# Kernel tuning notes

Hardware: AMD Instinct MI355X
Metric: run time of the kernel (lower is better)

The kernel has to match this reference:

```python
import jax, jax.numpy as jnp
import numpy as np

B, N, D, H = 64, 257, 1024, 16
HD = D // H  # 64


def setup_inputs() -> dict:
    key = jax.random.key(0)
    k1, k2, k3, k4, k5, k6 = jax.random.split(key, 6)
    x = jax.random.normal(k1, (B, N, D), dtype=jnp.float32)
    # boolean key mask per batch; never mask CLS token (col 0) so no fully-masked rows
    mask = jax.random.randint(k2, (B, N), 0, 2) > 0
    mask = mask.at[:, 0].set(False)
    s = 1.0 / np.sqrt(D)
    in_proj_w = jax.random.normal(k3, (3 * D, D), dtype=jnp.float32) * s
    in_proj_b = jax.random.normal(k4, (3 * D,), dtype=jnp.float32) * 0.02
    out_proj_w = jax.random.normal(k5, (D, D), dtype=jnp.float32) * s
    out_proj_b = jax.random.normal(k6, (D,), dtype=jnp.float32) * 0.02
    return {"x": x, "mask": mask, "in_proj_w": in_proj_w, "in_proj_b": in_proj_b,
            "out_proj_w": out_proj_w, "out_proj_b": out_proj_b}


def reference(x, mask, in_proj_w, in_proj_b, out_proj_w, out_proj_b):
    b, n, d = x.shape
    h, hd = H, d // H
    # fused QKV projection: [b, n, 3*d]
    qkv = jnp.einsum('bnd,ed->bne', x, in_proj_w) + in_proj_b
    # einops 'b n (qkv h d) -> qkv b h n d'
    qkv = qkv.reshape(b, n, 3, h, hd).transpose(2, 0, 3, 1, 4)
    q, k, v = qkv[0], qkv[1], qkv[2]  # each [b, h, n, hd]
    attn_weights = jnp.einsum('bhqe,bhke->bhqk', q, k) / jnp.sqrt(jnp.asarray(hd, x.dtype))
    # mode == 'mask': -inf on masked keys (broadcast over heads and queries)
    attn_weights = jnp.where(mask[:, None, None, :], -jnp.inf, attn_weights)
    attn_matrix = jax.nn.softmax(attn_weights, axis=-1)
    out = jnp.einsum('bhqk,bhke->bhqe', attn_matrix, v)  # [b, h, n, hd]
    out = out.transpose(0, 2, 1, 3).reshape(b, n, d)      # 'b h n d -> b n (h d)'
    return jnp.einsum('bnd,ed->bne', out, out_proj_w) + out_proj_b
```

## Files before the change

kernel.cpp:

```cpp
#include <hip/hip_runtime.h>

#define B_   64
#define N_   257
#define D_   1024
#define H_   16
#define HD_  64
#define M_   (B_*N_)
#define CK_  96
#define VTS_ 128
#define PLS_ 104

typedef __bf16 bf16x8 __attribute__((ext_vector_type(8)));
typedef __bf16 bf16x4 __attribute__((ext_vector_type(4)));
typedef float  f32x4  __attribute__((ext_vector_type(4)));

__device__ __forceinline__ void gload_lds16(const void* g, void* l) {
    __builtin_amdgcn_global_load_lds(
        (const __attribute__((address_space(1))) void*)g,
        (__attribute__((address_space(3))) void*)l, 16, 0, 0);
}

#define XQ_  4210688
#define W1Q_ 786432
#define W2Q_ 262144
__global__ __launch_bounds__(256) void cvt_all(const float* __restrict__ x,
                                               const float* __restrict__ w1,
                                               const float* __restrict__ w2,
                                               __bf16* __restrict__ xb,
                                               __bf16* __restrict__ w1b,
                                               __bf16* __restrict__ w2b) {
    int i = blockIdx.x * 256 + threadIdx.x;
    const float* src; __bf16* dst; int j;
    if (i < XQ_) { src = x; dst = xb; j = i; }
    else if (i < XQ_ + W1Q_) { src = w1; dst = w1b; j = i - XQ_; }
    else if (i < XQ_ + W1Q_ + W2Q_) { src = w2; dst = w2b; j = i - XQ_ - W1Q_; }
    else return;
    float4 v = reinterpret_cast<const float4*>(src)[j];
    bf16x4 o;
    o[0] = (__bf16)v.x; o[1] = (__bf16)v.y; o[2] = (__bf16)v.z; o[3] = (__bf16)v.w;
    *reinterpret_cast<bf16x4*>(dst + (size_t)j * 4) = o;
}

__global__ __launch_bounds__(256) void qkv_gemm(const __bf16* __restrict__ A,
                                                const __bf16* __restrict__ W,
                                                const float* __restrict__ bias,
                                                __bf16* __restrict__ qw,
                                                __bf16* __restrict__ kw,
                                                __bf16* __restrict__ vw) {
    __shared__ __align__(16) char smem[32768];
    __bf16* As = (__bf16*)smem;
    __bf16* Ws = (__bf16*)(smem + 16384);
    __bf16* Ct = (__bf16*)smem;
    const int bid = blockIdx.x;
    int rowt, colt;
    if (bid < 3072) {
        const int xcd = bid & 7, idx = bid >> 3;
        colt = idx >> 4;
        rowt = xcd * 16 + (idx & 15);
    } else {
        rowt = 128; colt = bid - 3072;
    }
    const int row0 = rowt * 128, col0 = colt * 128;
    const int tid  = threadIdx.x;
    const int lane = tid & 63, wv = tid >> 6;
    const int wm = (wv >> 1) * 64, wn = (wv & 1) * 64;
    const int fr = lane & 15, fq = lane >> 4;
    size_t sA[4], sW[4];
#pragma unroll
    for (int i = 0; i < 4; ++i) {
        const int c = tid + i * 256;
        const int r = c >> 3, g = (c & 7) ^ (r & 7);
        sA[i] = (size_t)(row0 + r) * 1024 + g * 8;
        sW[i] = (size_t)(col0 + r) * 1024 + g * 8;
    }
    f32x4 acc[4][4] = {};
    for (int k0 = 0; k0 < 1024; k0 += 64) {
#pragma unroll
        for (int i = 0; i < 4; ++i) {
            gload_lds16(A + sA[i] + k0, (char*)As + i * 4096 + wv * 1024);
            gload_lds16(W + sW[i] + k0, (char*)Ws + i * 4096 + wv * 1024);
        }
        __syncthreads();
#pragma unroll
        for (int ks = 0; ks < 2; ++ks) {
            const int goff = (((ks * 4 + fq) ^ (fr & 7)) * 8);
            bf16x8 af[4], bw[4];
#pragma unroll
            for (int i = 0; i < 4; ++i)
                af[i] = *reinterpret_cast<const bf16x8*>(&As[(wm + i * 16 + fr) * 64 + goff]);
#pragma unroll
            for (int j = 0; j < 4; ++j)
                bw[j] = *reinterpret_cast<const bf16x8*>(&Ws[(wn + j * 16 + fr) * 64 + goff]);
#pragma unroll
            for (int i = 0; i < 4; ++i)
#pragma unroll
                for (int j = 0; j < 4; ++j)
                    acc[i][j] = __builtin_amdgcn_mfma_f32_16x16x32_bf16(af[i], bw[j], acc[i][j], 0, 0, 0);
        }
        __syncthreads();
    }
    const int which = col0 >> 10;
    __bf16* dst = which == 0 ? qw : (which == 1 ? kw : vw);
    const float scale = which == 0 ? 0.125f : 1.0f;
    float bj[4];
#pragma unroll
    for (int j = 0; j < 4; ++j) bj[j] = bias[col0 + wn + j * 16 + fr];
#pragma unroll
    for (int i = 0; i < 4; ++i)
#pragma unroll
        for (int r = 0; r < 4; ++r) {
            const int row = wm + i * 16 + fq * 4 + r;
#pragma unroll
            for (int j = 0; j < 4; ++j)
                Ct[row * 128 + wn + j * 16 + fr] = (__bf16)((acc[i][j][r] + bj[j]) * scale);
        }
    __syncthreads();
    const int h0 = (col0 >> 6) & 15;
    const int col = (tid & 15) * 8;
    const int h = h0 + (col >> 6), hd = col & 63;
#pragma unroll
    for (int p = 0; p < 8; ++p) {
        const int row = p * 16 + (tid >> 4);
        const int m = row0 + row;
        if (m < M_) {
            bf16x8 v = *reinterpret_cast<const bf16x8*>(&Ct[row * 128 + col]);
            const int bb = m / 257, nn = m - bb * 257;
            *reinterpret_cast<bf16x8*>(dst + ((size_t)(bb * 16 + h) * 257 + nn) * 64 + hd) = v;
        }
    }
}

__global__ __launch_bounds__(256) void attn_kernel(const __bf16* __restrict__ qw,
                                                   const __bf16* __restrict__ kw,
                                                   const __bf16* __restrict__ vw,
                                                   const int* __restrict__ mask,
                                                   __bf16* __restrict__ attn) {
    const int bh = blockIdx.x;
    const int bb = bh >> 4, hh = bh & 15;
    const int q0 = blockIdx.y * 64;
    const int tid = threadIdx.x, lane = tid & 63, wv = tid >> 6;
    const int fr = lane & 15, fq = lane >> 4;
    const float NEG_INF = -__builtin_inff();

    __shared__ __align__(16) __bf16 Qs[64 * 64];
    __shared__ __align__(16) __bf16 Ks[CK_ * 64];
    __shared__ __align__(16) __bf16 Vt[64 * VTS_];
    __shared__ __align__(16) __bf16 Pl[4][16 * PLS_];
    __shared__ float maskb[288];

    const __bf16* qg = qw + ((size_t)bh * 257 + q0) * 64;
    const __bf16* kg = kw + (size_t)bh * 257 * 64;
    const __bf16* vg = vw + (size_t)bh * 257 * 64;
    const int* mg = mask + bb * 257;

    for (int idx = tid; idx < 288; idx += 256)
        maskb[idx] = (idx < 257 && mg[idx] == 0) ? 0.0f : NEG_INF;

#pragma unroll
    for (int i = 0; i < 2; ++i) {
        const int c = tid + i * 256;
        const int r = c >> 3, g = (c & 7) ^ (r & 7);
        gload_lds16(qg + (size_t)r * 64 + g * 8, (char*)Qs + i * 4096 + wv * 1024);
    }

    float m_run[4] = {NEG_INF, NEG_INF, NEG_INF, NEG_INF};
    float l_run[4] = {};
    f32x4 Oa[4] = {};

    for (int c3 = 0; c3 < 3; ++c3) {
        const int k0 = c3 * CK_;
        __syncthreads();
#pragma unroll
        for (int i = 0; i < 3; ++i) {
            const int c = tid + i * 256;
            const int r = c >> 3, g = (c & 7) ^ (r & 7);
            if (k0 + r < 257)
                gload_lds16(kg + (size_t)(k0 + r) * 64 + g * 8, (char*)Ks + i * 4096 + wv * 1024);
        }
#pragma unroll
        for (int it = 0; it < 3; ++it) {
            const int t = tid + it * 256;
            const int key = t >> 3, grp = t & 7;
            if (k0 + key < 257) {
                bf16x8 v8 = *reinterpret_cast<const bf16x8*>(vg + (size_t)(k0 + key) * 64 + grp * 8);
#pragma unroll
                for (int u = 0; u < 8; ++u) {
                    const int hd = grp * 8 + u;
                    Vt[hd * VTS_ + (((key >> 3) ^ (hd & 7)) * 8) + (key & 7)] = v8[u];
                }
            }
        }
        __syncthreads();

        f32x4 s[6];
        {
            bf16x8 aq[2];
#pragma unroll
            for (int ks = 0; ks < 2; ++ks)
                aq[ks] = *reinterpret_cast<const bf16x8*>(
                    &Qs[(wv * 16 + fr) * 64 + (((ks * 4 + fq) ^ (fr & 7)) * 8)]);
#pragma unroll
            for (int nt = 0; nt < 6; ++nt) {
                f32x4 sa = {};
#pragma unroll
                for (int ks = 0; ks < 2; ++ks) {
                    bf16x8 bk = *reinterpret_cast<const bf16x8*>(
                        &Ks[(nt * 16 + fr) * 64 + (((ks * 4 + fq) ^ (fr & 7)) * 8)]);
                    sa = __builtin_amdgcn_mfma_f32_16x16x32_bf16(aq[ks], bk, sa, 0, 0, 0);
                }
                const float mb = maskb[k0 + nt * 16 + fr];
#pragma unroll
                for (int r = 0; r < 4; ++r) sa[r] += mb;
                s[nt] = sa;
            }
        }
        float alpha[4];
#pragma unroll
        for (int r = 0; r < 4; ++r) {
            float v = s[0][r];
#pragma unroll
            for (int nt = 1; nt < 6; ++nt) v = fmaxf(v, s[nt][r]);
            v = fmaxf(v, __shfl_xor(v, 1));
            v = fmaxf(v, __shfl_xor(v, 2));
            v = fmaxf(v, __shfl_xor(v, 4));
            v = fmaxf(v, __shfl_xor(v, 8));
            const float mnew = fmaxf(m_run[r], v);
            alpha[r] = __expf(m_run[r] - mnew);
            m_run[r] = mnew;
        }
        float sm[4] = {};
#pragma unroll
        for (int nt = 0; nt < 6; ++nt)
#pragma unroll
            for (int r = 0; r < 4; ++r) {
                const float p = __expf(s[nt][r] - m_run[r]);
                s[nt][r] = p;
                sm[r] += p;
            }
#pragma unroll
        for (int r = 0; r < 4; ++r) {
            float v = sm[r];
            v += __shfl_xor(v, 1);
            v += __shfl_xor(v, 2);
            v += __shfl_xor(v, 4);
            v += __shfl_xor(v, 8);
            l_run[r] = l_run[r] * alpha[r] + v;
        }
#pragma unroll
        for (int ot = 0; ot < 4; ++ot)
#pragma unroll
            for (int r = 0; r < 4; ++r) Oa[ot][r] *= alpha[r];
#pragma unroll
        for (int nt = 0; nt < 6; ++nt)
#pragma unroll
            for (int r = 0; r < 4; ++r)
                Pl[wv][(fq * 4 + r) * PLS_ + nt * 16 + fr] = (__bf16)s[nt][r];
        __syncthreads();
        bf16x8 ap[3];
#pragma unroll
        for (int kk = 0; kk < 3; ++kk)
            ap[kk] = *reinterpret_cast<const bf16x8*>(&Pl[wv][fr * PLS_ + kk * 32 + fq * 8]);
#pragma unroll
        for (int ot = 0; ot < 4; ++ot) {
            const int row = ot * 16 + fr;
#pragma unroll
            for (int kk = 0; kk < 3; ++kk) {
                bf16x8 bv = *reinterpret_cast<const bf16x8*>(
                    &Vt[row * VTS_ + (((kk * 4 + fq) ^ (fr & 7)) * 8)]);
                Oa[ot] = __builtin_amdgcn_mfma_f32_16x16x32_bf16(ap[kk], bv, Oa[ot], 0, 0, 0);
            }
        }
    }
#pragma unroll
    for (int r = 0; r < 4; ++r) {
        const int n = q0 + wv * 16 + fq * 4 + r;
        const float inv = 1.0f / l_run[r];
#pragma unroll
        for (int ot = 0; ot < 4; ++ot)
            attn[((size_t)(bb * 257 + n)) * 1024 + hh * 64 + ot * 16 + fr] =
                (__bf16)(Oa[ot][r] * inv);
    }
}

__global__ __launch_bounds__(320) void attn_tail(const __bf16* __restrict__ qw,
                                                 const __bf16* __restrict__ kw,
                                                 const __bf16* __restrict__ vw,
                                                 const int* __restrict__ mask,
                                                 __bf16* __restrict__ attn) {
    const int bh = blockIdx.x;
    const int bb = bh >> 4, hh = bh & 15;
    const int tid = threadIdx.x, wv = tid >> 6;
    const float NEG_INF = -__builtin_inff();
    __shared__ float pbuf[257];
    __shared__ float red[5];
    __shared__ float gstat[2];

    const __bf16* qg = qw + ((size_t)bh * 257 + 256) * 64;
    const __bf16* kg = kw + (size_t)bh * 257 * 64;
    const __bf16* vg = vw + (size_t)bh * 257 * 64;

    float s = NEG_INF;
    if (tid < 257) {
        const __bf16* kr = kg + (size_t)tid * 64;
        float acc = 0.0f;
#pragma unroll
        for (int g = 0; g < 8; ++g) {
            bf16x8 qv = *reinterpret_cast<const bf16x8*>(qg + g * 8);
            bf16x8 kv = *reinterpret_cast<const bf16x8*>(kr + g * 8);
#pragma unroll
            for (int u = 0; u < 8; ++u) acc += (float)qv[u] * (float)kv[u];
        }
        s = (mask[bb * 257 + tid] == 0) ? acc : NEG_INF;
    }
    float v = s;
#pragma unroll
    for (int d = 1; d < 64; d <<= 1) v = fmaxf(v, __shfl_xor(v, d));
    if ((tid & 63) == 0) red[wv] = v;
    __syncthreads();
    if (tid == 0) {
        float m = red[0];
#pragma unroll
        for (int w = 1; w < 5; ++w) m = fmaxf(m, red[w]);
        gstat[0] = m;
    }
    __syncthreads();
    const float gmax = gstat[0];
    float p = (tid < 257) ? __expf(s - gmax) : 0.0f;
    if (tid < 257) pbuf[tid] = p;
    float sv = p;
#pragma unroll
    for (int d = 1; d < 64; d <<= 1) sv += __shfl_xor(sv, d);
    if ((tid & 63) == 0) red[wv] = sv;
    __syncthreads();
    if (tid == 0) gstat[1] = red[0] + red[1] + red[2] + red[3] + red[4];
    __syncthreads();
    if (tid < 64) {
        const float inv = 1.0f / gstat[1];
        float o = 0.0f;
        for (int j = 0; j < 257; ++j)
            o += pbuf[j] * (float)vg[(size_t)j * 64 + tid];
        attn[((size_t)(bb * 257 + 256)) * 1024 + hh * 64 + tid] = (__bf16)(o * inv);
    }
}

__global__ __launch_bounds__(256) void out_gemm(const __bf16* __restrict__ A,
                                                const __bf16* __restrict__ W,
                                                const float* __restrict__ bias,
                                                float* __restrict__ out) {
    __shared__ __align__(16) char smem[32768];
    __bf16* As = (__bf16*)smem;
    __bf16* Ws = (__bf16*)(smem + 16384);
    const int bid = blockIdx.x;
    int rowt, colt;
    if (bid < 1024) {
        const int xcd = bid & 7, idx = bid >> 3;
        colt = idx >> 4;
        rowt = xcd * 16 + (idx & 15);
    } else {
        rowt = 128; colt = bid - 1024;
    }
    const int row0 = rowt * 128, col0 = colt * 128;
    const int tid  = threadIdx.x;
    const int lane = tid & 63, wv = tid >> 6;
    const int wm = (wv >> 1) * 64, wn = (wv & 1) * 64;
    const int fr = lane & 15, fq = lane >> 4;
    size_t sA[4], sW[4];
#pragma unroll
    for (int i = 0; i < 4; ++i) {
        const int c = tid + i * 256;
        const int r = c >> 3, g = (c & 7) ^ (r & 7);
        sA[i] = (size_t)(row0 + r) * 1024 + g * 8;
        sW[i] = (size_t)(col0 + r) * 1024 + g * 8;
    }
    f32x4 acc[4][4] = {};
    for (int k0 = 0; k0 < 1024; k0 += 64) {
#pragma unroll
        for (int i = 0; i < 4; ++i) {
            gload_lds16(A + sA[i] + k0, (char*)As + i * 4096 + wv * 1024);
            gload_lds16(W + sW[i] + k0, (char*)Ws + i * 4096 + wv * 1024);
        }
        __syncthreads();
#pragma unroll
        for (int ks = 0; ks < 2; ++ks) {
            const int goff = (((ks * 4 + fq) ^ (fr & 7)) * 8);
            bf16x8 af[4], bw[4];
#pragma unroll
            for (int i = 0; i < 4; ++i)
                af[i] = *reinterpret_cast<const bf16x8*>(&As[(wm + i * 16 + fr) * 64 + goff]);
#pragma unroll
            for (int j = 0; j < 4; ++j)
                bw[j] = *reinterpret_cast<const bf16x8*>(&Ws[(wn + j * 16 + fr) * 64 + goff]);
#pragma unroll
            for (int i = 0; i < 4; ++i)
#pragma unroll
                for (int j = 0; j < 4; ++j)
                    acc[i][j] = __builtin_amdgcn_mfma_f32_16x16x32_bf16(af[i], bw[j], acc[i][j], 0, 0, 0);
        }
        __syncthreads();
    }
    float bj[4];
#pragma unroll
    for (int j = 0; j < 4; ++j) bj[j] = bias[col0 + wn + j * 16 + fr];
#pragma unroll
    for (int i = 0; i < 4; ++i)
#pragma unroll
        for (int r = 0; r < 4; ++r) {
            const int m = row0 + wm + i * 16 + fq * 4 + r;
            if (m < M_) {
                float* p = out + (size_t)m * 1024 + col0 + wn + fr;
#pragma unroll
                for (int j = 0; j < 4; ++j) p[j * 16] = acc[i][j][r] + bj[j];
            }
        }
}

extern "C" void kernel_launch(void* const* d_in, const int* in_sizes, int n_in,
                              void* d_out, int out_size, void* d_ws, size_t ws_size,
                              hipStream_t stream) {
    const float* x  = (const float*)d_in[0];
    const int* mask = (const int*)d_in[1];
    const float* w1 = (const float*)d_in[2];
    const float* b1 = (const float*)d_in[3];
    const float* w2 = (const float*)d_in[4];
    const float* b2 = (const float*)d_in[5];
    float* out = (float*)d_out;
    char* ws = (char*)d_ws;
    __bf16* x_bf  = (__bf16*)(ws);
    __bf16* w1_bf = (__bf16*)(ws + 33816576);
    __bf16* w2_bf = (__bf16*)(ws + 40108032);
    __bf16* q_ws  = (__bf16*)(ws + 42205184);
    __bf16* k_ws  = (__bf16*)(ws + 75890688);
    __bf16* v_ws  = (__bf16*)(ws + 109576192);
    __bf16* a_bf  = (__bf16*)(ws + 143261696);

    cvt_all<<<20544, 256, 0, stream>>>(x, w1, w2, x_bf, w1_bf, w2_bf);
    qkv_gemm<<<3096, 256, 0, stream>>>(x_bf, w1_bf, b1, q_ws, k_ws, v_ws);
    attn_kernel<<<dim3(1024, 4), 256, 0, stream>>>(q_ws, k_ws, v_ws, mask, a_bf);
    attn_tail<<<1024, 320, 0, stream>>>(q_ws, k_ws, v_ws, mask, a_bf);
    out_gemm<<<1032, 256, 0, stream>>>(a_bf, w2_bf, b2, out);
}
```

Measured before the change: 455.0 us.

## Replace both GEMMs with double-buffered 256x256 tile GEMM template

Both projection GEMMs are replaced by one templated kernel using 256x256 tiles, 512 threads, 128KB of LDS in two ping-pong buffers, and a split prefetch interleaved with MFMA quadrants under explicit barriers, vmcnt waits and setprio. Blocks are remapped so each XCD gets a contiguous range of tiles. The aim is to raise data reuse per tile and overlap global loads with compute, removing the load-then-sync stall of the old single-buffered 128x128 kernels. In exchange, 128KB LDS per block limits occupancy, the grids are small (780 and 260 blocks) which can leave CUs idle in the last wave, and the hand-placed waits and barriers risk races.

```diff
diff --git a/kernel.cpp b/kernel.cpp
--- a/kernel.cpp
+++ b/kernel.cpp
@@ -19,6 +19,10 @@
         (const __attribute__((address_space(1))) void*)g,
         (__attribute__((address_space(3))) void*)l, 16, 0, 0);
 }
+
+#define MEMF() asm volatile("" ::: "memory")
+#define BARRIER() do { MEMF(); __builtin_amdgcn_s_barrier(); MEMF(); } while (0)
+#define WAITV(n) asm volatile("s_waitcnt vmcnt(" #n ")" ::: "memory")
 
 #define XQ_  4210688
 #define W1Q_ 786432
@@ -41,93 +45,183 @@
     *reinterpret_cast<bf16x4*>(dst + (size_t)j * 4) = o;
 }
 
-__global__ __launch_bounds__(256) void qkv_gemm(const __bf16* __restrict__ A,
-                                                const __bf16* __restrict__ W,
-                                                const float* __restrict__ bias,
-                                                __bf16* __restrict__ qw,
-                                                __bf16* __restrict__ kw,
-                                                __bf16* __restrict__ vw) {
-    __shared__ __align__(16) char smem[32768];
-    __bf16* As = (__bf16*)smem;
-    __bf16* Ws = (__bf16*)(smem + 16384);
-    __bf16* Ct = (__bf16*)smem;
-    const int bid = blockIdx.x;
-    int rowt, colt;
-    if (bid < 3072) {
-        const int xcd = bid & 7, idx = bid >> 3;
-        colt = idx >> 4;
-        rowt = xcd * 16 + (idx & 15);
+template<int NT, int MODE>
+__global__ __launch_bounds__(512, 2) void gemm256(const __bf16* __restrict__ A,
+                                                  const __bf16* __restrict__ W,
+                                                  const float* __restrict__ bias,
+                                                  __bf16* __restrict__ qo,
+                                                  __bf16* __restrict__ ko,
+                                                  __bf16* __restrict__ vo,
+                                                  float* __restrict__ fo) {
+    __shared__ __align__(16) char smem[131072];
+    constexpr int NWG = 65 * NT;
+    constexpr int qd = NWG >> 3, rm = NWG & 7;
+    const int orig = blockIdx.x;
+    const int xcd = orig & 7, loc = orig >> 3;
+    const int wgid = (xcd < rm ? xcd * (qd + 1) : rm * (qd + 1) + (xcd - rm) * qd) + loc;
+    const int rowt = wgid / NT, colt = wgid - rowt * NT;
+    const int row0 = rowt * 256, col0 = colt * 256;
+
+    const int tid = threadIdx.x, lane = tid & 63, wv = tid >> 6;
+    const int wm = wv >> 2, wn = wv & 3;
+    const int fr = lane & 15, fq = lane >> 4, frs = lane & 7;
+
+    const int pr = tid >> 3;
+    const int pg = ((tid & 7) ^ (pr & 7)) * 8;
+    int srcA[4];
+    {
+        const int prow[4] = {0, 128, 64, 192};
+#pragma unroll
+        for (int p = 0; p < 4; ++p) {
+            int rg = row0 + prow[p] + pr;
+            if (rg > M_ - 1) rg = M_ - 1;
+            srcA[p] = rg * 1024 + pg;
+        }
+    }
+    int srcW[2], ldsW[2];
+#pragma unroll
+    for (int e = 0; e < 2; ++e) {
+        const int wb = (wv >> 1) * 64 + e * 16 + (wv & 1) * 8;
+        srcW[e] = (col0 + wb + (lane >> 3)) * 1024 + pg;
+        ldsW[e] = wb * 128;
+    }
+    char* const At0 = smem;
+    char* const At1 = smem + 32768;
+    char* const Wt0 = smem + 65536;
+    char* const Wt1 = smem + 98304;
+
+#define STG_AF(dst, kk) do { gload_lds16(A + srcA[0] + (kk), (dst) + wv * 1024); \
+                             gload_lds16(A + srcA[1] + (kk), (dst) + 16384 + wv * 1024); } while (0)
+#define STG_AB(dst, kk) do { gload_lds16(A + srcA[2] + (kk), (dst) + 8192 + wv * 1024); \
+                             gload_lds16(A + srcA[3] + (kk), (dst) + 24576 + wv * 1024); } while (0)
+#define STG_WF(dst, kk) do { gload_lds16(W + srcW[0] + (kk), (dst) + ldsW[0]); \
+                             gload_lds16(W + srcW[1] + (kk), (dst) + ldsW[1]); } while (0)
+#define STG_WB(dst, kk) do { gload_lds16(W + srcW[0] + 32768 + (kk), (dst) + ldsW[0] + 4096); \
+                             gload_lds16(W + srcW[1] + 32768 + (kk), (dst) + ldsW[1] + 4096); } while (0)
+#define LD_A(buf, rqo) do { \
+    _Pragma("unroll") for (int i = 0; i < 4; ++i) \
+    _Pragma("unroll") for (int ks = 0; ks < 2; ++ks) \
+        af[i][ks] = *(const bf16x8*)((buf) + (wm * 128 + (rqo) + i * 16 + fr) * 128 \
+                                           + (((ks * 4 + fq) ^ frs) << 4)); \
+} while (0)
+#define LD_B(buf, co, bw) do { \
+    _Pragma("unroll") for (int j = 0; j < 2; ++j) \
+    _Pragma("unroll") for (int ks = 0; ks < 2; ++ks) \
+        bw[j][ks] = *(const bf16x8*)((buf) + (wn * 64 + (co) + j * 16 + fr) * 128 \
+                                           + (((ks * 4 + fq) ^ frs) << 4)); \
+} while (0)
+#define MFMA_Q(i0, j0, bw) do { \
+    __builtin_amdgcn_s_setprio(1); \
+    _Pragma("unroll") for (int i = 0; i < 4; ++i) \
+    _Pragma("unroll") for (int j = 0; j < 2; ++j) \
+    _Pragma("unroll") for (int ks = 0; ks < 2; ++ks) \
+        acc[(i0) + i][(j0) + j] = __builtin_amdgcn_mfma_f32_16x16x32_bf16( \
+            af[i][ks], bw[j][ks], acc[(i0) + i][(j0) + j], 0, 0, 0); \
+    __builtin_amdgcn_s_setprio(0); \
+} while (0)
+
+    f32x4 acc[8][4] = {};
+    bf16x8 af[4][2], bw0[2][2], bw1[2][2];
+
+    STG_AF(At0, 0); STG_WF(Wt0, 0); STG_WB(Wt0, 0); STG_AB(At0, 0);
+    WAITV(4);
+    BARRIER();
+
+#pragma unroll 2
+    for (int t = 0; t < 16; ++t) {
+        char* const Ac = (t & 1) ? At1 : At0;
+        char* const Wc = (t & 1) ? Wt1 : Wt0;
+        char* const An = (t & 1) ? At0 : At1;
+        char* const Wn = (t & 1) ? Wt0 : Wt1;
+        const int kk = (t < 15) ? (t + 1) * 64 : 960;
+        LD_A(Ac, 0);
+        LD_B(Wc, 0, bw0);
+        STG_AF(An, kk);
+        WAITV(4);
+        BARRIER();
+        MFMA_Q(0, 0, bw0);
+        BARRIER();
+        LD_B(Wc, 32, bw1);
+        STG_WF(Wn, kk);
+        WAITV(4);
+        BARRIER();
+        MFMA_Q(0, 2, bw1);
+        BARRIER();
+        LD_A(Ac, 64);
+        STG_WB(Wn, kk);
+        BARRIER();
+        MFMA_Q(4, 2, bw1);
+        BARRIER();
+        STG_AB(An, kk);
+        WAITV(4);
+        BARRIER();
+        MFMA_Q(4, 0, bw0);
+        BARRIER();
+    }
+    WAITV(0);
+    BARRIER();
+
+    if constexpr (MODE == 0) {
+        const int which = colt >> 2;
+        __bf16* const dst = which == 0 ? qo : (which == 1 ? ko : vo);
+        const float scale = which == 0 ? 0.125f : 1.0f;
+        float bj[4];
+#pragma unroll
+        for (int j = 0; j < 4; ++j) bj[j] = bias[col0 + wn * 64 + j * 16 + fr];
+        __bf16* const Ct = (__bf16*)smem;
+#pragma unroll
+        for (int i = 0; i < 8; ++i) {
+            const int rb = wm * 128 + (i >> 2) * 64 + (i & 3) * 16 + fq * 4;
+#pragma unroll
+            for (int r = 0; r < 4; ++r) {
+                const int row = rb + r;
+#pragma unroll
+                for (int j = 0; j < 4; ++j) {
+                    const int cu = wn * 64 + j * 16 + fr;
+                    Ct[row * 256 + (((cu >> 3) ^ (row & 7)) * 8) + (cu & 7)] =
+                        (__bf16)((acc[i][j][r] + bj[j]) * scale);
+                }
+            }
+        }
+        BARRIER();
+#pragma unroll
+        for (int p = 0; p < 16; ++p) {
+            const int row = p * 16 + (tid >> 5);
+            const int m = row0 + row;
+            if (m < M_) {
+                const int gl = tid & 31;
+                bf16x8 v = *(const bf16x8*)(Ct + row * 256 + ((gl ^ (row & 7)) * 8));
+                const int cG = col0 + gl * 8;
+                const int h = (cG >> 6) & 15, hd = cG & 63;
+                const int bb = m / 257, nn = m - bb * 257;
+                *reinterpret_cast<bf16x8*>(dst + ((size_t)(bb * 16 + h) * 257 + nn) * 64 + hd) = v;
+            }
+        }
     } else {
-        rowt = 128; colt = bid - 3072;
-    }
-    const int row0 = rowt * 128, col0 = colt * 128;
-    const int tid  = threadIdx.x;
-    const int lane = tid & 63, wv = tid >> 6;
-    const int wm = (wv >> 1) * 64, wn = (wv & 1) * 64;
-    const int fr = lane & 15, fq = lane >> 4;
-    size_t sA[4], sW[4];
-#pragma unroll
-    for (int i = 0; i < 4; ++i) {
-        const int c = tid + i * 256;
-        const int r = c >> 3, g = (c & 7) ^ (r & 7);
-        sA[i] = (size_t)(row0 + r) * 1024 + g * 8;
-        sW[i] = (size_t)(col0 + r) * 1024 + g * 8;
-    }
-    f32x4 acc[4][4] = {};
-    for (int k0 = 0; k0 < 1024; k0 += 64) {
-#pragma unroll
-        for (int i = 0; i < 4; ++i) {
-            gload_lds16(A + sA[i] + k0, (char*)As + i * 4096 + wv * 1024);
-            gload_lds16(W + sW[i] + k0, (char*)Ws + i * 4096 + wv * 1024);
-        }
-        __syncthreads();
-#pragma unroll
-        for (int ks = 0; ks < 2; ++ks) {
-            const int goff = (((ks * 4 + fq) ^ (fr & 7)) * 8);
-            bf16x8 af[4], bw[4];
-#pragma unroll
-            for (int i = 0; i < 4; ++i)
-                af[i] = *reinterpret_cast<const bf16x8*>(&As[(wm + i * 16 + fr) * 64 + goff]);
-#pragma unroll
-            for (int j = 0; j < 4; ++j)
-                bw[j] = *reinterpret_cast<const bf16x8*>(&Ws[(wn + j * 16 + fr) * 64 + goff]);
-#pragma unroll
-            for (int i = 0; i < 4; ++i)
-#pragma unroll
-                for (int j = 0; j < 4; ++j)
-                    acc[i][j] = __builtin_amdgcn_mfma_f32_16x16x32_bf16(af[i], bw[j], acc[i][j], 0, 0, 0);
-        }
-        __syncthreads();
-    }
-    const int which = col0 >> 10;
-    __bf16* dst = which == 0 ? qw : (which == 1 ? kw : vw);
-    const float scale = which == 0 ? 0.125f : 1.0f;
-    float bj[4];
-#pragma unroll
-    for (int j = 0; j < 4; ++j) bj[j] = bias[col0 + wn + j * 16 + fr];
-#pragma unroll
-    for (int i = 0; i < 4; ++i)
-#pragma unroll
-        for (int r = 0; r < 4; ++r) {
-            const int row = wm + i * 16 + fq * 4 + r;
-#pragma unroll
-            for (int j = 0; j < 4; ++j)
-                Ct[row * 128 + wn + j * 16 + fr] = (__bf16)((acc[i][j][r] + bj[j]) * scale);
-        }
-    __syncthreads();
-    const int h0 = (col0 >> 6) & 15;
-    const int col = (tid & 15) * 8;
-    const int h = h0 + (col >> 6), hd = col & 63;
-#pragma unroll
-    for (int p = 0; p < 8; ++p) {
-        const int row = p * 16 + (tid >> 4);
-        const int m = row0 + row;
-        if (m < M_) {
-            bf16x8 v = *reinterpret_cast<const bf16x8*>(&Ct[row * 128 + col]);
-            const int bb = m / 257, nn = m - bb * 257;
-            *reinterpret_cast<bf16x8*>(dst + ((size_t)(bb * 16 + h) * 257 + nn) * 64 + hd) = v;
-        }
-    }
+        float bj[4];
+#pragma unroll
+        for (int j = 0; j < 4; ++j) bj[j] = bias[col0 + wn * 64 + j * 16 + fr];
+#pragma unroll
+        for (int i = 0; i < 8; ++i) {
+            const int rb = wm * 128 + (i >> 2) * 64 + (i & 3) * 16 + fq * 4;
+#pragma unroll
+            for (int r = 0; r < 4; ++r) {
+                const int m = row0 + rb + r;
+                if (m < M_) {
+                    float* const p = fo + (size_t)m * 1024 + col0 + wn * 64 + fr;
+#pragma unroll
+                    for (int j = 0; j < 4; ++j) p[j * 16] = acc[i][j][r] + bj[j];
+                }
+            }
+        }
+    }
+#undef STG_AF
+#undef STG_AB
+#undef STG_WF
+#undef STG_WB
+#undef LD_A
+#undef LD_B
+#undef MFMA_Q
 }
 
 __global__ __launch_bounds__(256) void attn_kernel(const __bf16* __restrict__ qw,
@@ -341,77 +435,6 @@
             o += pbuf[j] * (float)vg[(size_t)j * 64 + tid];
         attn[((size_t)(bb * 257 + 256)) * 1024 + hh * 64 + tid] = (__bf16)(o * inv);
     }
-}
-
-__global__ __launch_bounds__(256) void out_gemm(const __bf16* __restrict__ A,
-                                                const __bf16* __restrict__ W,
-                                                const float* __restrict__ bias,
-                                                float* __restrict__ out) {
-    __shared__ __align__(16) char smem[32768];
-    __bf16* As = (__bf16*)smem;
-    __bf16* Ws = (__bf16*)(smem + 16384);
-    const int bid = blockIdx.x;
-    int rowt, colt;
-    if (bid < 1024) {
-        const int xcd = bid & 7, idx = bid >> 3;
-        colt = idx >> 4;
-        rowt = xcd * 16 + (idx & 15);
-    } else {
-        rowt = 128; colt = bid - 1024;
-    }
-    const int row0 = rowt * 128, col0 = colt * 128;
-    const int tid  = threadIdx.x;
-    const int lane = tid & 63, wv = tid >> 6;
-    const int wm = (wv >> 1) * 64, wn = (wv & 1) * 64;
-    const int fr = lane & 15, fq = lane >> 4;
-    size_t sA[4], sW[4];
-#pragma unroll
-    for (int i = 0; i < 4; ++i) {
-        const int c = tid + i * 256;
-        const int r = c >> 3, g = (c & 7) ^ (r & 7);
-        sA[i] = (size_t)(row0 + r) * 1024 + g * 8;
-        sW[i] = (size_t)(col0 + r) * 1024 + g * 8;
-    }
-    f32x4 acc[4][4] = {};
-    for (int k0 = 0; k0 < 1024; k0 += 64) {
-#pragma unroll
-        for (int i = 0; i < 4; ++i) {
-            gload_lds16(A + sA[i] + k0, (char*)As + i * 4096 + wv * 1024);
-            gload_lds16(W + sW[i] + k0, (char*)Ws + i * 4096 + wv * 1024);
-        }
-        __syncthreads();
-#pragma unroll
-        for (int ks = 0; ks < 2; ++ks) {
-            const int goff = (((ks * 4 + fq) ^ (fr & 7)) * 8);
-            bf16x8 af[4], bw[4];
-#pragma unroll
-            for (int i = 0; i < 4; ++i)
-                af[i] = *reinterpret_cast<const bf16x8*>(&As[(wm + i * 16 + fr) * 64 + goff]);
-#pragma unroll
-            for (int j = 0; j < 4; ++j)
-                bw[j] = *reinterpret_cast<const bf16x8*>(&Ws[(wn + j * 16 + fr) * 64 + goff]);
-#pragma unroll
-            for (int i = 0; i < 4; ++i)
-#pragma unroll
-                for (int j = 0; j < 4; ++j)
-                    acc[i][j] = __builtin_amdgcn_mfma_f32_16x16x32_bf16(af[i], bw[j], acc[i][j], 0, 0, 0);
-        }
-        __syncthreads();
-    }
-    float bj[4];
-#pragma unroll
-    for (int j = 0; j < 4; ++j) bj[j] = bias[col0 + wn + j * 16 + fr];
-#pragma unroll
-    for (int i = 0; i < 4; ++i)
-#pragma unroll
-        for (int r = 0; r < 4; ++r) {
-            const int m = row0 + wm + i * 16 + fq * 4 + r;
-            if (m < M_) {
-                float* p = out + (size_t)m * 1024 + col0 + wn + fr;
-#pragma unroll
-                for (int j = 0; j < 4; ++j) p[j * 16] = acc[i][j][r] + bj[j];
-            }
-        }
 }
 
 extern "C" void kernel_launch(void* const* d_in, const int* in_sizes, int n_in,
@@ -434,8 +457,8 @@
     __bf16* a_bf  = (__bf16*)(ws + 143261696);
 
     cvt_all<<<20544, 256, 0, stream>>>(x, w1, w2, x_bf, w1_bf, w2_bf);
-    qkv_gemm<<<3096, 256, 0, stream>>>(x_bf, w1_bf, b1, q_ws, k_ws, v_ws);
+    gemm256<12, 0><<<780, 512, 0, stream>>>(x_bf, w1_bf, b1, q_ws, k_ws, v_ws, nullptr);
     attn_kernel<<<dim3(1024, 4), 256, 0, stream>>>(q_ws, k_ws, v_ws, mask, a_bf);
     attn_tail<<<1024, 320, 0, stream>>>(q_ws, k_ws, v_ws, mask, a_bf);
-    out_gemm<<<1032, 256, 0, stream>>>(a_bf, w2_bf, b2, out);
-}
+    gemm256<4, 1><<<260, 512, 0, stream>>>(a_bf, w2_bf, b2, nullptr, nullptr, nullptr, out);
+}
```

After: 428.7 us. 1.06x faster.
